# Kernel optimization log

Hardware: AMD Instinct MI355X
Metric: run time of the kernel (lower is better)

Reference implementation:

```python
import jax, jax.numpy as jnp
import numpy as np

B, I, J, C, H = 1, 384, 384, 128, 4
CH = 128          # overall hidden
HD = CH // H      # 32 per head
INF = 1000000000.0
EPS = 1e-5


def setup_inputs() -> dict:
    key = jax.random.key(0)
    ks = jax.random.split(key, 10)
    s = 0.02
    return {
        "x": jax.random.normal(ks[0], (B, I, J, C), dtype=jnp.float32),
        "mask": jnp.ones((B, I, J), dtype=jnp.float32),
        "ln_w": jnp.ones((C,), dtype=jnp.float32),
        "ln_b": jnp.zeros((C,), dtype=jnp.float32),
        "wz": jax.random.normal(ks[1], (C, H), dtype=jnp.float32) * s,
        "bz": jnp.zeros((H,), dtype=jnp.float32),
        "wq": jax.random.normal(ks[2], (C, CH), dtype=jnp.float32) * s,
        "wk": jax.random.normal(ks[3], (C, CH), dtype=jnp.float32) * s,
        "wv": jax.random.normal(ks[4], (C, CH), dtype=jnp.float32) * s,
        "wg": jax.random.normal(ks[5], (C, CH), dtype=jnp.float32) * s,
        "bg": jnp.ones((CH,), dtype=jnp.float32),
        "wo": jax.random.normal(ks[6], (CH, C), dtype=jnp.float32) * s,
        "bo": jnp.zeros((C,), dtype=jnp.float32),
    }


def _layer_norm(x, w, b):
    mu = jnp.mean(x, axis=-1, keepdims=True)
    var = jnp.mean(jnp.square(x - mu), axis=-1, keepdims=True)
    return (x - mu) * jax.lax.rsqrt(var + EPS) * w + b


def reference(x, mask, ln_w, ln_b, wz, bz, wq, wk, wv, wg, bg, wo, bo):
    # starting=True: attention over last row axis J
    x = _layer_norm(x, ln_w, ln_b)                      # [B,I,J,C]
    mask_bias = (INF * (mask - 1.0))[:, :, None, None, :]   # [B,I,1,1,J]
    # triangle bias: linear_z then permute (2,0,1), unsqueeze(-4) -> [B,1,H,I,J]
    tri_bias = jnp.einsum("bijc,ch->bhij", x, wz) + bz[None, :, None, None]
    tri_bias = tri_bias[:, None]                        # [B,1,H,I,J]

    q = jnp.einsum("bijc,cd->bijd", x, wq).reshape(B, I, J, H, HD)
    k = jnp.einsum("bijc,cd->bijd", x, wk).reshape(B, I, J, H, HD)
    v = jnp.einsum("bijc,cd->bijd", x, wv).reshape(B, I, J, H, HD)
    q = q / jnp.sqrt(jnp.float32(HD))

    a = jnp.einsum("biqhd,bikhd->bihqk", q, k)          # [B,I,H,J,J]
    a = a + mask_bias + tri_bias
    a = jax.nn.softmax(a, axis=-1)
    o = jnp.einsum("bihqk,bikhd->biqhd", a, v)          # [B,I,J,H,HD]

    g = jax.nn.sigmoid(jnp.einsum("bijc,cd->bijd", x, wg) + bg)
    o = o.reshape(B, I, J, CH) * g
    return jnp.einsum("bijd,dc->bijc", o, wo) + bo      # [B,I,J,C]
```

## Files before the change

kernel.cpp:

```cpp
#include <hip/hip_runtime.h>
#include <math.h>

#define I_DIM 384
#define C_DIM 128
#define H_NUM 4
#define HD_DIM 32
#define M_DIM (I_DIM*I_DIM)
#define INF_F 1000000000.0f
#define EPS_F 1e-5f
#define QSCALE 0.17677669529663687f
#define LOG2E_F 1.4426950408889634f

typedef __attribute__((ext_vector_type(8))) short short8;
typedef __attribute__((ext_vector_type(4))) float f32x4;
union U4S8 { uint4 u; short8 s; };

__device__ __forceinline__ unsigned short f2bf(float f) {
    unsigned int u = __float_as_uint(f);
    u += 0x7fffu + ((u >> 16) & 1u);
    return (unsigned short)(u >> 16);
}
__device__ __forceinline__ float bf2f(unsigned short h) {
    return __uint_as_float((unsigned int)h << 16);
}
__device__ __forceinline__ unsigned int pk2(float a, float b) {
    return (unsigned int)f2bf(a) | ((unsigned int)f2bf(b) << 16);
}
__device__ __forceinline__ unsigned int cvtpk(float lo, float hi) {
    unsigned int r;
    asm("v_cvt_pk_bf16_f32 %0, %1, %2" : "=v"(r) : "v"(lo), "v"(hi));
    return r;
}

__device__ uint4 wfmt_dev[5*4096];

__device__ __forceinline__ void load_lds16(const uint4* gp, void* lp) {
    __builtin_amdgcn_global_load_lds(
        (const __attribute__((address_space(1))) unsigned int*)gp,
        (__attribute__((address_space(3))) unsigned int*)lp,
        16, 0, 0);
}

__global__ __launch_bounds__(256) void wprep_kernel(
    const float* __restrict__ wq, const float* __restrict__ wk,
    const float* __restrict__ wg, const float* __restrict__ wv,
    const float* __restrict__ wo)
{
    const int tid  = blockIdx.x*256 + threadIdx.x;
    const int l    = tid & 63, tile = tid >> 6;
    const int ks   = tile & 3, nt = (tile >> 2) & 7;
    const int s    = (tile >> 5) & 1, m = tile >> 6;
    const float* W = (m==0)?wq:(m==1)?wk:(m==2)?wg:(m==3)?wv:wo;
    const float scale = (m==0) ? QSCALE*LOG2E_F : 1.f;
    const int n  = nt*16 + (l & 15);
    const int kb = ks*32 + (l >> 4)*8;
    unsigned int hw[4];
    #pragma unroll
    for (int jp = 0; jp < 4; ++jp) {
        unsigned short hs[2];
        #pragma unroll
        for (int e = 0; e < 2; ++e) {
            float v = W[(size_t)(kb + jp*2 + e)*C_DIM + n] * scale;
            unsigned short h = f2bf(v);
            if (s) h = f2bf(v - bf2f(h));
            hs[e] = h;
        }
        hw[jp] = (unsigned int)hs[0] | ((unsigned int)hs[1] << 16);
    }
    wfmt_dev[(size_t)m*4096 + (size_t)((s*8 + nt)*4 + ks)*64 + l] =
        make_uint4(hw[0], hw[1], hw[2], hw[3]);
}

__global__ __launch_bounds__(256, 3) void ln_proj_kernel(
    const float* __restrict__ x,
    const float* __restrict__ lnw, const float* __restrict__ lnb,
    const float* __restrict__ wz,  const float* __restrict__ bz,
    const float* __restrict__ bg,
    float* __restrict__ qo, unsigned short* __restrict__ ko16,
    unsigned int* __restrict__ vto, float* __restrict__ go,
    float* __restrict__ zo)
{
    __shared__ __align__(16) unsigned int xs[4096];
    __shared__ __align__(16) uint4 wbuf4[2048];
    unsigned int* vts = xs;

    const int t    = threadIdx.x;
    const int row0 = blockIdx.x * 64;
    const int w = t >> 6, l = t & 63, n16 = l & 15, quad = l >> 4;

    #pragma unroll
    for (int it = 0; it < 4; ++it) {
        const int tl = w*4 + it;
        const int s = tl >> 3, ntl = (tl >> 2) & 1, ks = tl & 3;
        load_lds16(wfmt_dev + (size_t)((s*8 + ntl)*4 + ks)*64 + l,
                   (char*)wbuf4 + tl*1024);
    }

    float4 xv[8];
    const int r = t >> 2, qt = t & 3, c0 = qt * 32;
    const int sw = (r & 7) << 2;
    {
        const float* xrow = x + (size_t)(row0 + r)*C_DIM + c0;
        float s = 0.f, ss = 0.f;
        #pragma unroll
        for (int i2 = 0; i2 < 8; i2++) {
            xv[i2] = ((const float4*)xrow)[i2];
            s  += xv[i2].x + xv[i2].y + xv[i2].z + xv[i2].w;
            ss += xv[i2].x*xv[i2].x + xv[i2].y*xv[i2].y
                + xv[i2].z*xv[i2].z + xv[i2].w*xv[i2].w;
        }
        s  += __shfl_xor(s, 1);  s  += __shfl_xor(s, 2);
        ss += __shfl_xor(ss, 1); ss += __shfl_xor(ss, 2);
        const float mean = s * (1.f/128.f);
        const float var  = ss * (1.f/128.f) - mean*mean;
        const float rstd = rsqrtf(var + EPS_F);
        const float4* wz4 = (const float4*)wz;
        float4 zacc = make_float4(0.f,0.f,0.f,0.f);
        #pragma unroll
        for (int i2 = 0; i2 < 8; i2++) {
            float4 w4 = ((const float4*)(lnw + c0))[i2];
            float4 b4 = ((const float4*)(lnb + c0))[i2];
            float4 r4;
            r4.x = (xv[i2].x - mean)*rstd*w4.x + b4.x;
            r4.y = (xv[i2].y - mean)*rstd*w4.y + b4.y;
            r4.z = (xv[i2].z - mean)*rstd*w4.z + b4.z;
            r4.w = (xv[i2].w - mean)*rstd*w4.w + b4.w;
            const float4 za = wz4[c0 + i2*4 + 0];
            const float4 zb_ = wz4[c0 + i2*4 + 1];
            const float4 zc = wz4[c0 + i2*4 + 2];
            const float4 zd = wz4[c0 + i2*4 + 3];
            zacc.x += r4.x*za.x + r4.y*zb_.x + r4.z*zc.x + r4.w*zd.x;
            zacc.y += r4.x*za.y + r4.y*zb_.y + r4.z*zc.y + r4.w*zd.y;
            zacc.z += r4.x*za.z + r4.y*zb_.z + r4.z*zc.z + r4.w*zd.z;
            zacc.w += r4.x*za.w + r4.y*zb_.w + r4.z*zc.w + r4.w*zd.w;
            const int wi = r*64 + qt*16 + i2*2;
            xs[(wi  ) ^ sw] = pk2(r4.x, r4.y);
            xs[(wi+1) ^ sw] = pk2(r4.z, r4.w);
            xv[i2] = r4;
        }
        zacc.x += __shfl_xor(zacc.x, 1); zacc.x += __shfl_xor(zacc.x, 2);
        zacc.y += __shfl_xor(zacc.y, 1); zacc.y += __shfl_xor(zacc.y, 2);
        zacc.z += __shfl_xor(zacc.z, 1); zacc.z += __shfl_xor(zacc.z, 2);
        zacc.w += __shfl_xor(zacc.w, 1); zacc.w += __shfl_xor(zacc.w, 2);
        const float zv = (qt==0)?zacc.x:(qt==1)?zacc.y:(qt==2)?zacc.z:zacc.w;
        zo[(size_t)qt*M_DIM + row0 + r] = (zv + bz[qt]) * LOG2E_F;
    }
    __syncthreads();

    U4S8 ah[4], al[4];
    const int arow = w*16 + n16;
    #pragma unroll
    for (int ks = 0; ks < 4; ++ks) {
        const int bofs = arow*256 + ((ks*64 + quad*16) ^ ((arow & 7) << 4));
        ah[ks].u = *(const uint4*)((const char*)xs + bofs);
    }
    __syncthreads();

    #pragma unroll
    for (int i2 = 0; i2 < 8; i2++) {
        const float4 r4 = xv[i2];
        const unsigned short h0 = f2bf(r4.x), h1 = f2bf(r4.y),
                             h2 = f2bf(r4.z), h3 = f2bf(r4.w);
        const int wi = r*64 + qt*16 + i2*2;
        xs[(wi  ) ^ sw] = (unsigned int)f2bf(r4.x - bf2f(h0))
                        | ((unsigned int)f2bf(r4.y - bf2f(h1)) << 16);
        xs[(wi+1) ^ sw] = (unsigned int)f2bf(r4.z - bf2f(h2))
                        | ((unsigned int)f2bf(r4.w - bf2f(h3)) << 16);
    }
    __syncthreads();
    #pragma unroll
    for (int ks = 0; ks < 4; ++ks) {
        const int bofs = arow*256 + ((ks*64 + quad*16) ^ ((arow & 7) << 4));
        al[ks].u = *(const uint4*)((const char*)xs + bofs);
    }

    const int i_blk = row0 / I_DIM;
    const int jp0   = (row0 % I_DIM) >> 1;
    const int rw0   = row0 + w*16 + quad*4;

    int p = 0;
    #pragma unroll
    for (int rd = 0; rd < 16; ++rd) {
        const int mi = rd >> 2, qq = rd & 3;

        if (rd < 15) {
            const int m2 = (rd+1) >> 2, q2 = (rd+1) & 3;
            #pragma unroll
            for (int it = 0; it < 4; ++it) {
                const int tl = w*4 + it;
                const int s = tl >> 3, ntl2 = (tl >> 2) & 1, ks = tl & 3;
                load_lds16(wfmt_dev + (size_t)m2*4096
                           + (size_t)((s*8 + (q2*2 + ntl2))*4 + ks)*64 + l,
                           (char*)wbuf4 + (p^1)*16384 + tl*1024);
            }
        }

        f32x4 acc[2];
        #pragma unroll
        for (int ntl = 0; ntl < 2; ++ntl) {
            f32x4 a = {0.f, 0.f, 0.f, 0.f};
            #pragma unroll
            for (int ks = 0; ks < 4; ++ks) {
                U4S8 bh, bl;
                bh.u = wbuf4[p*1024 + (    ntl*4 + ks)*64 + l];
                bl.u = wbuf4[p*1024 + (8 + ntl*4 + ks)*64 + l];
                a = __builtin_amdgcn_mfma_f32_16x16x32_bf16(ah[ks].s, bh.s, a, 0,0,0);
                a = __builtin_amdgcn_mfma_f32_16x16x32_bf16(al[ks].s, bh.s, a, 0,0,0);
                a = __builtin_amdgcn_mfma_f32_16x16x32_bf16(ah[ks].s, bl.s, a, 0,0,0);
            }
            acc[ntl] = a;
        }

        if (mi == 0) {
            #pragma unroll
            for (int ntl = 0; ntl < 2; ++ntl)
                #pragma unroll
                for (int rr = 0; rr < 4; ++rr)
                    qo[(size_t)(rw0 + rr)*C_DIM + qq*32 + ntl*16 + n16] =
                        acc[ntl][rr];
        } else if (mi == 1) {
            #pragma unroll
            for (int ntl = 0; ntl < 2; ++ntl)
                #pragma unroll
                for (int rr = 0; rr < 4; ++rr)
                    ko16[(size_t)(rw0 + rr)*C_DIM + qq*32 + ntl*16 + n16] =
                        f2bf(acc[ntl][rr]);
        } else if (mi == 2) {
            #pragma unroll
            for (int ntl = 0; ntl < 2; ++ntl) {
                const float bgv = bg[qq*32 + ntl*16 + n16];
                #pragma unroll
                for (int rr = 0; rr < 4; ++rr)
                    go[(size_t)(rw0 + rr)*C_DIM + qq*32 + ntl*16 + n16] =
                        1.f/(1.f + __expf(-(acc[ntl][rr] + bgv)));
            }
        } else {
            #pragma unroll
            for (int ntl = 0; ntl < 2; ++ntl)
                #pragma unroll
                for (int pr = 0; pr < 2; ++pr)
                    vts[(ntl*16 + n16)*33 + w*8 + quad*2 + pr] =
                        pk2(acc[ntl][2*pr], acc[ntl][2*pr+1]);
            __syncthreads();
            for (int idx = t; idx < 32*32; idx += 256) {
                const int ch_l = idx >> 5, pp = idx & 31;
                vto[((size_t)i_blk*C_DIM + qq*32 + ch_l)*192 + jp0 + pp] =
                    vts[ch_l*33 + pp];
            }
        }

        __syncthreads();
        p ^= 1;
    }
}

__global__ __launch_bounds__(256, 3) void attn_mfma_kernel(
    const float* q, const unsigned short* __restrict__ k16,
    const unsigned int* __restrict__ vt32, const float* __restrict__ zb,
    const float* __restrict__ mask, float* o)
{
    __shared__ uint4 Ks4[384*4];
    __shared__ uint4 VTl[32*49];
    __shared__ __align__(16) float mbl[384];

    const int ii = blockIdx.x;
    const int h  = blockIdx.y;
    const int t  = threadIdx.x;
    const size_t rbase = (size_t)ii*I_DIM*C_DIM + h*HD_DIM;

    for (int idx = t; idx < 1536; idx += 256) {
        const int j = idx >> 2, c4 = idx & 3;
        Ks4[j*4 + (c4 ^ ((j >> 1) & 3))] =
            ((const uint4*)k16)[rbase/8 + (size_t)j*16 + c4];
    }
    for (int idx = t; idx < 1536; idx += 256) {
        const int d = idx / 48, m = idx - d*48;
        VTl[d*49 + m] = ((const uint4*)vt32)[((size_t)ii*C_DIM + h*HD_DIM + d)*48 + m];
    }
    for (int jj = t; jj < 384; jj += 256)
        mbl[jj] = (INF_F*LOG2E_F) * (mask[(size_t)ii*I_DIM + jj] - 1.f);
    __syncthreads();

    const int w = t >> 6, l = t & 63;
    const int n16 = l & 15, quad = l >> 4;
    const int slA = n16 + ((quad & 1) << 5);
    const int slB = slA + 16;
    const bool hi = (quad & 2) != 0;

    #pragma unroll 1
    for (int qt = 0; qt < 6; qt++) {
        const int qg = w*6 + qt;

        U4S8 a;
        {
            const float* qrow = q + rbase + (size_t)(qg*16 + n16)*C_DIM + quad*8;
            const float4 f0 = ((const float4*)qrow)[0];
            const float4 f1 = ((const float4*)qrow)[1];
            a.u = make_uint4(cvtpk(f0.x,f0.y), cvtpk(f0.z,f0.w),
                             cvtpk(f1.x,f1.y), cvtpk(f1.z,f1.w));
        }

        f32x4 oacc0 = {0.f,0.f,0.f,0.f}, oacc1 = {0.f,0.f,0.f,0.f};
        float lsum = 0.f;
        const float* zrow = zb + (size_t)h*M_DIM
                          + (size_t)(qg*16 + n16)*I_DIM + quad*4;

        #pragma unroll 1
        for (int c = 0; c < 4; c++) {
            float4 zc4[6];
            #pragma unroll
            for (int k6 = 0; k6 < 6; k6++)
                zc4[k6] = *(const float4*)&zrow[96*c + k6*16];
            float4 mb4[6];
            #pragma unroll
            for (int k6 = 0; k6 < 6; k6++)
                mb4[k6] = *(const float4*)&mbl[96*c + k6*16 + quad*4];

            f32x4 accS[6];
            #pragma unroll
            for (int k6 = 0; k6 < 6; k6++) {
                const int key = (6*c + k6)*16 + n16;
                U4S8 b;
                b.u = Ks4[key*4 + (quad ^ ((key >> 1) & 3))];
                accS[k6] = __builtin_amdgcn_mfma_f32_16x16x32_bf16(
                    b.s, a.s, (f32x4){0.f,0.f,0.f,0.f}, 0, 0, 0);
            }

            unsigned int pu[6][2];
            #pragma unroll
            for (int k6 = 0; k6 < 6; k6++) {
                const float e0 = __builtin_amdgcn_exp2f(accS[k6][0] + zc4[k6].x + mb4[k6].x);
                const float e1 = __builtin_amdgcn_exp2f(accS[k6][1] + zc4[k6].y + mb4[k6].y);
                const float e2 = __builtin_amdgcn_exp2f(accS[k6][2] + zc4[k6].z + mb4[k6].z);
                const float e3 = __builtin_amdgcn_exp2f(accS[k6][3] + zc4[k6].w + mb4[k6].w);
                lsum += (e0 + e1) + (e2 + e3);
                pu[k6][0] = cvtpk(e0, e1);
                pu[k6][1] = cvtpk(e2, e3);
            }

            #pragma unroll
            for (int km = 0; km < 3; km++) {
                const unsigned int x0 = __shfl((int)pu[2*km  ][0], slA);
                const unsigned int x1 = __shfl((int)pu[2*km+1][0], slA);
                const unsigned int y0 = __shfl((int)pu[2*km  ][1], slA);
                const unsigned int y1 = __shfl((int)pu[2*km+1][1], slA);
                const unsigned int z0 = __shfl((int)pu[2*km  ][0], slB);
                const unsigned int z1 = __shfl((int)pu[2*km+1][0], slB);
                const unsigned int w0 = __shfl((int)pu[2*km  ][1], slB);
                const unsigned int w1 = __shfl((int)pu[2*km+1][1], slB);
                U4S8 pa;
                pa.u = make_uint4(hi?x1:x0, hi?y1:y0, hi?z1:z0, hi?w1:w0);
                U4S8 vb0, vb1;
                vb0.u = VTl[(n16     )*49 + quad + 4*km + 12*c];
                vb1.u = VTl[(16 + n16)*49 + quad + 4*km + 12*c];
                oacc0 = __builtin_amdgcn_mfma_f32_16x16x32_bf16(vb0.s, pa.s, oacc0, 0,0,0);
                oacc1 = __builtin_amdgcn_mfma_f32_16x16x32_bf16(vb1.s, pa.s, oacc1, 0,0,0);
            }
        }

        float s_ = lsum;
        s_ += __shfl_xor(s_, 16);
        s_ += __shfl_xor(s_, 32);
        const float rcp = 1.f / s_;
        const size_t orow = rbase + (size_t)(qg*16 + n16)*C_DIM;
        float4 o0 = make_float4(oacc0[0]*rcp, oacc0[1]*rcp,
                                oacc0[2]*rcp, oacc0[3]*rcp);
        float4 o1 = make_float4(oacc1[0]*rcp, oacc1[1]*rcp,
                                oacc1[2]*rcp, oacc1[3]*rcp);
        *(float4*)&o[orow + quad*4]      = o0;
        *(float4*)&o[orow + 16 + quad*4] = o1;
    }
}

__global__ __launch_bounds__(256, 3) void out_proj_kernel(
    const float* __restrict__ o, const float* g,
    const float* __restrict__ bo, float* out)
{
    __shared__ __align__(16) unsigned int xs[4096];
    __shared__ __align__(16) uint4 wbuf4[2048];
    const int t    = threadIdx.x;
    const int row0 = blockIdx.x * 64;
    const int w = t >> 6, l = t & 63, n16 = l & 15, quad = l >> 4;

    #pragma unroll
    for (int it = 0; it < 4; ++it) {
        const int tl = w*4 + it;
        const int s = tl >> 3, ntl = (tl >> 2) & 1, ks = tl & 3;
        load_lds16(wfmt_dev + (size_t)4*4096 + (size_t)((s*8 + ntl)*4 + ks)*64 + l,
                   (char*)wbuf4 + tl*1024);
    }

    float4 pv[8];
    const int r = t >> 2, qt = t & 3, c0 = qt * 32;
    const int sw = (r & 7) << 2;
    {
        const float4* orow = (const float4*)(o + (size_t)(row0 + r)*C_DIM + c0);
        const float4* grow = (const float4*)(g + (size_t)(row0 + r)*C_DIM + c0);
        #pragma unroll
        for (int i2 = 0; i2 < 8; i2++) {
            const float4 a = orow[i2];
            const float4 b = grow[i2];
            float4 p;
            p.x = a.x*b.x; p.y = a.y*b.y; p.z = a.z*b.z; p.w = a.w*b.w;
            const int wi = r*64 + qt*16 + i2*2;
            xs[(wi  ) ^ sw] = pk2(p.x, p.y);
            xs[(wi+1) ^ sw] = pk2(p.z, p.w);
            pv[i2] = p;
        }
    }
    __syncthreads();

    U4S8 ah[4], al[4];
    const int arow = w*16 + n16;
    #pragma unroll
    for (int ks = 0; ks < 4; ++ks) {
        const int bofs = arow*256 + ((ks*64 + quad*16) ^ ((arow & 7) << 4));
        ah[ks].u = *(const uint4*)((const char*)xs + bofs);
    }
    __syncthreads();
    #pragma unroll
    for (int i2 = 0; i2 < 8; i2++) {
        const float4 p = pv[i2];
        const unsigned short h0 = f2bf(p.x), h1 = f2bf(p.y),
                             h2 = f2bf(p.z), h3 = f2bf(p.w);
        const int wi = r*64 + qt*16 + i2*2;
        xs[(wi  ) ^ sw] = (unsigned int)f2bf(p.x - bf2f(h0))
                        | ((unsigned int)f2bf(p.y - bf2f(h1)) << 16);
        xs[(wi+1) ^ sw] = (unsigned int)f2bf(p.z - bf2f(h2))
                        | ((unsigned int)f2bf(p.w - bf2f(h3)) << 16);
    }
    __syncthreads();
    #pragma unroll
    for (int ks = 0; ks < 4; ++ks) {
        const int bofs = arow*256 + ((ks*64 + quad*16) ^ ((arow & 7) << 4));
        al[ks].u = *(const uint4*)((const char*)xs + bofs);
    }

    const int rw0 = row0 + w*16 + quad*4;
    int p = 0;
    #pragma unroll
    for (int qq = 0; qq < 4; ++qq) {
        if (qq < 3) {
            const int q2 = qq + 1;
            #pragma unroll
            for (int it = 0; it < 4; ++it) {
                const int tl = w*4 + it;
                const int s = tl >> 3, ntl2 = (tl >> 2) & 1, ks = tl & 3;
                load_lds16(wfmt_dev + (size_t)4*4096
                           + (size_t)((s*8 + (q2*2 + ntl2))*4 + ks)*64 + l,
                           (char*)wbuf4 + (p^1)*16384 + tl*1024);
            }
        }
        f32x4 acc[2];
        #pragma unroll
        for (int ntl = 0; ntl < 2; ++ntl) {
            f32x4 a = {0.f, 0.f, 0.f, 0.f};
            #pragma unroll
            for (int ks = 0; ks < 4; ++ks) {
                U4S8 bh, bl;
                bh.u = wbuf4[p*1024 + (    ntl*4 + ks)*64 + l];
                bl.u = wbuf4[p*1024 + (8 + ntl*4 + ks)*64 + l];
                a = __builtin_amdgcn_mfma_f32_16x16x32_bf16(ah[ks].s, bh.s, a, 0,0,0);
                a = __builtin_amdgcn_mfma_f32_16x16x32_bf16(al[ks].s, bh.s, a, 0,0,0);
                a = __builtin_amdgcn_mfma_f32_16x16x32_bf16(ah[ks].s, bl.s, a, 0,0,0);
            }
            acc[ntl] = a;
        }
        #pragma unroll
        for (int ntl = 0; ntl < 2; ++ntl) {
            const int n = qq*32 + ntl*16 + n16;
            const float bov = bo[n];
            #pragma unroll
            for (int rr = 0; rr < 4; ++rr)
                out[(size_t)(rw0 + rr)*C_DIM + n] = acc[ntl][rr] + bov;
        }
        __syncthreads();
        p ^= 1;
    }
}

extern "C" void kernel_launch(void* const* d_in, const int* in_sizes, int n_in,
                              void* d_out, int out_size, void* d_ws, size_t ws_size,
                              hipStream_t stream)
{
    (void)in_sizes; (void)n_in; (void)out_size; (void)ws_size;
    const float* x    = (const float*)d_in[0];
    const float* mask = (const float*)d_in[1];
    const float* lnw  = (const float*)d_in[2];
    const float* lnb  = (const float*)d_in[3];
    const float* wz   = (const float*)d_in[4];
    const float* bz   = (const float*)d_in[5];
    const float* wq   = (const float*)d_in[6];
    const float* wk   = (const float*)d_in[7];
    const float* wv   = (const float*)d_in[8];
    const float* wg   = (const float*)d_in[9];
    const float* bg   = (const float*)d_in[10];
    const float* wo   = (const float*)d_in[11];
    const float* bo   = (const float*)d_in[12];

    float* ws = (float*)d_ws;
    float* qb   = ws;
    float* zbuf = qb + (size_t)M_DIM*C_DIM;
    unsigned short* kb16 = (unsigned short*)(zbuf + (size_t)H_NUM*M_DIM);
    unsigned int*   vt32 = (unsigned int*)(kb16 + (size_t)M_DIM*C_DIM);
    float* gbuf = (float*)d_out;

    wprep_kernel<<<80, 256, 0, stream>>>(wq, wk, wg, wv, wo);
    ln_proj_kernel<<<M_DIM/64, 256, 0, stream>>>(
        x, lnw, lnb, wz, bz, bg, qb, kb16, vt32, gbuf, zbuf);
    attn_mfma_kernel<<<dim3(I_DIM, H_NUM), 256, 0, stream>>>(
        qb, kb16, vt32, zbuf, mask, qb );
    out_proj_kernel<<<M_DIM/64, 256, 0, stream>>>(
        qb, gbuf, bo, (float*)d_out);
}
```

Measured before the change: 435.9 us.

## Fold bias into MFMA accumulator init, add setprio, unroll chunk loop

```diff
diff --git a/kernel.cpp b/kernel.cpp
--- a/kernel.cpp
+++ b/kernel.cpp
@@ -305,34 +305,38 @@
         const float* zrow = zb + (size_t)h*M_DIM
                           + (size_t)(qg*16 + n16)*I_DIM + quad*4;
 
-        #pragma unroll 1
+        #pragma unroll 2
         for (int c = 0; c < 4; c++) {
-            float4 zc4[6];
-            #pragma unroll
-            for (int k6 = 0; k6 < 6; k6++)
-                zc4[k6] = *(const float4*)&zrow[96*c + k6*16];
-            float4 mb4[6];
-            #pragma unroll
-            for (int k6 = 0; k6 < 6; k6++)
-                mb4[k6] = *(const float4*)&mbl[96*c + k6*16 + quad*4];
+            f32x4 cin[6];
+            #pragma unroll
+            for (int k6 = 0; k6 < 6; k6++) {
+                const float4 z4 = *(const float4*)&zrow[96*c + k6*16];
+                const float4 m4 = *(const float4*)&mbl[96*c + k6*16 + quad*4];
+                cin[k6][0] = z4.x + m4.x;
+                cin[k6][1] = z4.y + m4.y;
+                cin[k6][2] = z4.z + m4.z;
+                cin[k6][3] = z4.w + m4.w;
+            }
 
             f32x4 accS[6];
+            __builtin_amdgcn_s_setprio(1);
             #pragma unroll
             for (int k6 = 0; k6 < 6; k6++) {
                 const int key = (6*c + k6)*16 + n16;
                 U4S8 b;
                 b.u = Ks4[key*4 + (quad ^ ((key >> 1) & 3))];
                 accS[k6] = __builtin_amdgcn_mfma_f32_16x16x32_bf16(
-                    b.s, a.s, (f32x4){0.f,0.f,0.f,0.f}, 0, 0, 0);
-            }
+                    b.s, a.s, cin[k6], 0, 0, 0);
+            }
+            __builtin_amdgcn_s_setprio(0);
 
             unsigned int pu[6][2];
             #pragma unroll
             for (int k6 = 0; k6 < 6; k6++) {
-                const float e0 = __builtin_amdgcn_exp2f(accS[k6][0] + zc4[k6].x + mb4[k6].x);
-                const float e1 = __builtin_amdgcn_exp2f(accS[k6][1] + zc4[k6].y + mb4[k6].y);
-                const float e2 = __builtin_amdgcn_exp2f(accS[k6][2] + zc4[k6].z + mb4[k6].z);
-                const float e3 = __builtin_amdgcn_exp2f(accS[k6][3] + zc4[k6].w + mb4[k6].w);
+                const float e0 = __builtin_amdgcn_exp2f(accS[k6][0]);
+                const float e1 = __builtin_amdgcn_exp2f(accS[k6][1]);
+                const float e2 = __builtin_amdgcn_exp2f(accS[k6][2]);
+                const float e3 = __builtin_amdgcn_exp2f(accS[k6][3]);
                 lsum += (e0 + e1) + (e2 + e3);
                 pu[k6][0] = cvtpk(e0, e1);
                 pu[k6][1] = cvtpk(e2, e3);
@@ -353,8 +357,10 @@
                 U4S8 vb0, vb1;
                 vb0.u = VTl[(n16     )*49 + quad + 4*km + 12*c];
                 vb1.u = VTl[(16 + n16)*49 + quad + 4*km + 12*c];
+                __builtin_amdgcn_s_setprio(1);
                 oacc0 = __builtin_amdgcn_mfma_f32_16x16x32_bf16(vb0.s, pa.s, oacc0, 0,0,0);
                 oacc1 = __builtin_amdgcn_mfma_f32_16x16x32_bf16(vb1.s, pa.s, oacc1, 0,0,0);
+                __builtin_amdgcn_s_setprio(0);
             }
         }
 
```

Result: no change. 435.9 us (+0.0%).
